# Performance work log

Measured on AMD Instinct MI355X. Metric: run time of the kernel, lower is better.

## Reference

```python
import jax, jax.numpy as jnp
import numpy as np
import math

H, D = 8, 128            # num_heads, head_dim (hidden=1024)
CHUNK, PAST, FUT = 12, 12, 0
CTX = CHUNK + PAST + FUT  # 24
SOFTCAP = 50.0
INVALID = 1e-09
Q_SCALE = D ** (-0.5) / math.log(2)
K_SCALE = math.log(1.0 + math.e) / math.log(2)


def setup_inputs() -> dict:
    key = jax.random.key(0)
    ks = jax.random.split(key, 7)
    B, S, HS = 16, 2400, 1024
    w = lambda k: jax.random.normal(k, (HS, HS), jnp.float32) * 0.02
    return {
        "x": jax.random.normal(ks[0], (B, S, HS), jnp.float32),
        "pos_emb": jax.random.normal(ks[1], (CTX + 1, HS), jnp.float32),
        "Wq": w(ks[2]),
        "Wk": w(ks[3]),
        "Wv": w(ks[4]),
        "Wpost": w(ks[5]),
        "Wrel": w(ks[6]),
        "per_dim_scale": jnp.zeros((D,), jnp.float32),
    }


def _to_blocks(t):
    # [B,S,H,D] -> [B,nb,CHUNK,H,D] (pad S up to multiple of CHUNK)
    B, S, h, d = t.shape
    nb = -(-S // CHUNK)
    t = jnp.pad(t, ((0, 0), (0, nb * CHUNK - S), (0, 0), (0, 0)))
    return t.reshape(B, nb, CHUNK, h, d)


def _block_context(t):
    # [B,S,H,D] -> [B,nb,CTX,H,D]: per-block window of PAST left context + chunk + FUT
    B, S, h, d = t.shape
    nb = -(-S // CHUNK)
    tp = jnp.pad(t, ((0, 0), (PAST, FUT + CHUNK - 1), (0, 0), (0, 0)))
    idx = jnp.arange(nb)[:, None] * CHUNK + jnp.arange(CTX)[None, :]  # [nb,CTX]
    return tp[:, idx]  # gather -> [B,nb,CTX,H,D]


def _rel_shift(x):
    # [B,H,nb,CHUNK,P] -> [B,H,nb,CHUNK,CTX] via Transformer-XL reshape trick
    B, h, nb, bs, P = x.shape
    x = jnp.pad(x, ((0, 0), (0, 0), (0, 0), (0, 0), (0, CTX + 1 - P)))
    x = x.reshape(B, h, nb, bs * (CTX + 1))[..., : bs * CTX]
    return x.reshape(B, h, nb, bs, CTX)


def reference(x, pos_emb, Wq, Wk, Wv, Wpost, Wrel, per_dim_scale):
    B, S, HS = x.shape
    q = (x @ Wq).reshape(B, S, H, D) * Q_SCALE * jax.nn.softplus(per_dim_scale)
    k = (x @ Wk).reshape(B, S, H, D) * K_SCALE
    v = (x @ Wv).reshape(B, S, H, D)

    qb = _to_blocks(q)        # [B,nb,CHUNK,H,D]
    kc = _block_context(k)    # [B,nb,CTX,H,D]
    vc = _block_context(v)    # [B,nb,CTX,H,D]
    nb = qb.shape[1]

    rel_k = (pos_emb @ Wrel).reshape(-1, H, D)  # [P,H,D]

    # content-content scores: [B,H,nb,CHUNK,CTX]
    matrix_ac = jnp.einsum('bnqhd,bnkhd->bhnqk', qb, kc)
    # content-position scores with rel-shift: [B,H,nb,CHUNK,P] -> [...,CTX]
    matrix_bd = jnp.einsum('bnqhd,phd->bhnqp', qb, rel_k)
    matrix_bd = _rel_shift(matrix_bd)

    attn = jnp.tanh((matrix_ac + matrix_bd) / SOFTCAP) * SOFTCAP
    attn = jax.nn.softmax(attn, axis=-1)

    out = jnp.einsum('bhnqk,bnkhd->bnqhd', attn, vc)  # [B,nb,CHUNK,H,D]
    out = out.reshape(B, nb * CHUNK, H * D)[:, :S, :]
    return out @ Wpost
```

## Files before the change

### kernel.cpp

```cpp
#include <hip/hip_runtime.h>
#include <hip/hip_bf16.h>
#include <cmath>

#define AS_GLOBAL __attribute__((address_space(1)))
#define AS_LDS    __attribute__((address_space(3)))

typedef __attribute__((ext_vector_type(8))) short bf16x8;
typedef __attribute__((ext_vector_type(4))) float f32x4;
typedef unsigned short u16;

__device__ __forceinline__ u16 f2bf(float f) {
  union { __hip_bfloat16 h; u16 u; } cv;
  cv.h = __float2bfloat16(f);
  return cv.u;
}
__device__ __forceinline__ float bf2f(u16 u) {
  union { unsigned u32; float f; } v;
  v.u32 = ((unsigned)u) << 16;
  return v.f;
}


__global__ void k_f32_to_bf16(const float* __restrict__ in, u16* __restrict__ out, int n4) {
  int i = blockIdx.x * 256 + threadIdx.x;
  if (i >= n4) return;
  float4 v = ((const float4*)in)[i];
  ushort4 o;
  o.x = f2bf(v.x); o.y = f2bf(v.y); o.z = f2bf(v.z); o.w = f2bf(v.w);
  ((ushort4*)out)[i] = o;
}

__global__ void k_transpose_w(const float* __restrict__ in, u16* __restrict__ out) {
  __shared__ float tile[32][33];
  const int tx = threadIdx.x & 31;
  const int ty = threadIdx.x >> 5;
  const int x0 = blockIdx.x * 32, y0 = blockIdx.y * 32;
  #pragma unroll
  for (int i = 0; i < 32; i += 8)
    tile[ty + i][tx] = in[(size_t)(y0 + ty + i) * 1024 + x0 + tx];
  __syncthreads();
  #pragma unroll
  for (int i = 0; i < 32; i += 8)
    out[(size_t)(x0 + ty + i) * 1024 + y0 + tx] = f2bf(tile[tx][ty + i]);
}

__global__ void k_qscale(const float* __restrict__ pds, float* __restrict__ qs, float qscale_c) {
  int n = blockIdx.x * 256 + threadIdx.x;
  float s = pds[n & 127];
  qs[n] = qscale_c * log1pf(expf(s));
}

__global__ void k_relk(const float* __restrict__ pos, const u16* __restrict__ wrt,
                       u16* __restrict__ relkb) {
  __shared__ float prow[1024];
  const int tid = threadIdx.x;
  const int p = blockIdx.y;
  ((float4*)prow)[tid] = ((const float4*)(pos + (size_t)p * 1024))[tid];
  __syncthreads();
  int nn = blockIdx.x * 256 + tid;
  const u16* wr = wrt + (size_t)nn * 1024;
  float acc = 0.f;
  for (int kk = 0; kk < 1024; kk += 8) {
    ushort4 u0 = *(const ushort4*)(wr + kk);
    ushort4 u1 = *(const ushort4*)(wr + kk + 4);
    acc += bf2f(u0.x) * prow[kk + 0] + bf2f(u0.y) * prow[kk + 1]
         + bf2f(u0.z) * prow[kk + 2] + bf2f(u0.w) * prow[kk + 3]
         + bf2f(u1.x) * prow[kk + 4] + bf2f(u1.y) * prow[kk + 5]
         + bf2f(u1.z) * prow[kk + 6] + bf2f(u1.w) * prow[kk + 7];
  }
  relkb[(size_t)p * 1024 + nn] = f2bf(acc);
}


#define BAR() __builtin_amdgcn_s_barrier()
#define VMCNT(n) asm volatile("s_waitcnt vmcnt(" #n ")" ::: "memory")

#define STAGE(d, t)                                                                       \
  do {                                                                                    \
    const int koff_ = (t) << 6;                                                           \
    _Pragma("unroll")                                                                     \
    for (int j_ = 0; j_ < 4; ++j_) {                                                      \
      int f_ = tid + j_ * 512;                                                            \
      int r_ = f_ >> 3;                                                                   \
      int cs_ = ((f_ & 7) ^ (r_ & 7)) << 3;                                               \
      __builtin_amdgcn_global_load_lds(                                                   \
          (const AS_GLOBAL u16*)(A + (size_t)(m0 + r_) * K + koff_ + cs_),                \
          (AS_LDS u16*)&lds[d][0][f_ << 3], 16, 0, 0);                                    \
      __builtin_amdgcn_global_load_lds(                                                   \
          (const AS_GLOBAL u16*)(Bt + (size_t)(n0 + r_) * K + koff_ + cs_),               \
          (AS_LDS u16*)&lds[d][1][f_ << 3], 16, 0, 0);                                    \
    }                                                                                     \
  } while (0)

#define COMPUTE(d)                                                                        \
  do {                                                                                    \
    bf16x8 bfr_[4][2];                                                                    \
    _Pragma("unroll")                                                                     \
    for (int ni_ = 0; ni_ < 4; ++ni_) {                                                   \
      int brow_ = wn * 64 + ni_ * 16 + l16;                                               \
      int bb_ = brow_ * 64, bx_ = brow_ & 7;                                              \
      bfr_[ni_][0] = *(const bf16x8*)&lds[d][1][bb_ + ((quad ^ bx_) << 3)];               \
      bfr_[ni_][1] = *(const bf16x8*)&lds[d][1][bb_ + (((4 + quad) ^ bx_) << 3)];         \
    }                                                                                     \
    __builtin_amdgcn_s_setprio(1);                                                        \
    _Pragma("unroll")                                                                     \
    for (int mi_ = 0; mi_ < 8; ++mi_) {                                                   \
      int arow_ = wm * 128 + mi_ * 16 + l16;                                              \
      int ab_ = arow_ * 64, ax_ = arow_ & 7;                                              \
      bf16x8 a0_ = *(const bf16x8*)&lds[d][0][ab_ + ((quad ^ ax_) << 3)];                 \
      bf16x8 a1_ = *(const bf16x8*)&lds[d][0][ab_ + (((4 + quad) ^ ax_) << 3)];           \
      _Pragma("unroll")                                                                   \
      for (int ni_ = 0; ni_ < 4; ++ni_) {                                                 \
        acc[mi_][ni_] =                                                                   \
            __builtin_amdgcn_mfma_f32_16x16x32_bf16(a0_, bfr_[ni_][0], acc[mi_][ni_], 0, 0, 0); \
        acc[mi_][ni_] =                                                                   \
            __builtin_amdgcn_mfma_f32_16x16x32_bf16(a1_, bfr_[ni_][1], acc[mi_][ni_], 0, 0, 0); \
      }                                                                                   \
    }                                                                                     \
    __builtin_amdgcn_s_setprio(0);                                                        \
  } while (0)

template <int OUTMODE>
__global__ __launch_bounds__(512, 2) void k_gemm256(
    const u16* __restrict__ A, const u16* __restrict__ Bt, void* __restrict__ Cout,
    const float* __restrict__ scale_vec, float scale_scalar, int M, int N, int K) {
  __shared__ __align__(16) u16 lds[2][2][16384];
  const int tid = threadIdx.x;
  const int wave = tid >> 6, lane = tid & 63;
  const int l16 = lane & 15, quad = lane >> 4;
  const int wm = wave >> 2, wn = wave & 3;

  const int q8 = (int)gridDim.x >> 3;
  const int wg = ((int)blockIdx.x & 7) * q8 + ((int)blockIdx.x >> 3);
  const int ntn = N >> 8;
  const int m0 = (wg / ntn) << 8;
  const int n0 = (wg % ntn) << 8;

  f32x4 acc[8][4];
  #pragma unroll
  for (int i = 0; i < 8; ++i)
    #pragma unroll
    for (int j = 0; j < 4; ++j) {
      f32x4 z = {0.f, 0.f, 0.f, 0.f};
      acc[i][j] = z;
    }

  STAGE(0, 0);
  STAGE(1, 1);
  VMCNT(8);
  BAR();

  const int nk = K >> 6;
  for (int i = 0; i + 2 < nk; i += 2) {
    COMPUTE(0);
    BAR();
    STAGE(0, i + 2);
    VMCNT(8);
    BAR();
    COMPUTE(1);
    BAR();
    STAGE(1, i + 3);
    VMCNT(8);
    BAR();
  }
  COMPUTE(0);
  VMCNT(0);
  BAR();
  COMPUTE(1);

  const int mb = m0 + wm * 128, nb = n0 + wn * 64;
  if (OUTMODE == 2) {
    u16* C = (u16*)Cout;
    #pragma unroll
    for (int ni = 0; ni < 4; ++ni) {
      int col = nb + ni * 16 + l16;
      #pragma unroll
      for (int mi = 0; mi < 8; ++mi) {
        int row = mb + mi * 16 + quad * 4;
        ushort4 o;
        o.x = f2bf(acc[mi][ni][0]);
        o.y = f2bf(acc[mi][ni][1]);
        o.z = f2bf(acc[mi][ni][2]);
        o.w = f2bf(acc[mi][ni][3]);
        *(ushort4*)&C[(size_t)col * M + row] = o;
      }
    }
  } else {
    #pragma unroll
    for (int ni = 0; ni < 4; ++ni) {
      int col = nb + ni * 16 + l16;
      float cs = scale_vec ? scale_vec[col] : scale_scalar;
      #pragma unroll
      for (int mi = 0; mi < 8; ++mi) {
        int row = mb + mi * 16 + quad * 4;
        #pragma unroll
        for (int r = 0; r < 4; ++r) {
          float v = acc[mi][ni][r] * cs;
          if (OUTMODE == 1)
            ((u16*)Cout)[(size_t)(row + r) * N + col] = f2bf(v);
          else
            ((float*)Cout)[(size_t)(row + r) * N + col] = v;
        }
      }
    }
  }
}

__global__ __launch_bounds__(256) void k_attn_mfma(
    const u16* __restrict__ q, const u16* __restrict__ k, const u16* __restrict__ vt,
    const u16* __restrict__ relkb, u16* __restrict__ ctx) {
  __shared__ float bdm_s[4][400];
  __shared__ u16 attnb[4][16 * 32];

  const int tid = threadIdx.x;
  const int w = tid >> 6, lane = tid & 63;
  const int l16 = lane & 15, quad = lane >> 4;
  const int id = blockIdx.x * 4 + w;
  const int b = id / 1600;
  const int rr = id % 1600;
  const int n = rr >> 3, h = rr & 7;
  const int s0 = n * 12;
  const size_t rowbase = (size_t)b * 2400;

  bf16x8 qf[4];
  {
    int sq = s0 + l16;
    if (sq > 2399) sq = 2399;
    const u16* qp = q + ((rowbase + sq) * 1024 + (size_t)h * 128 + quad * 8);
    #pragma unroll
    for (int c = 0; c < 4; ++c) qf[c] = *(const bf16x8*)(qp + 32 * c);
  }

  #pragma unroll
  for (int pt = 0; pt < 2; ++pt) {
    int p = pt * 16 + l16;
    const u16* rp = relkb + ((size_t)p * 1024 + (size_t)h * 128 + quad * 8);
    f32x4 acc = {0.f, 0.f, 0.f, 0.f};
    #pragma unroll
    for (int c = 0; c < 4; ++c)
      acc = __builtin_amdgcn_mfma_f32_16x16x32_bf16(qf[c], *(const bf16x8*)(rp + 32 * c), acc, 0, 0, 0);
    if (p < 25) {
      #pragma unroll
      for (int r = 0; r < 4; ++r)
        bdm_s[w][(quad * 4 + r) * 25 + p] = acc[r];
    }
  }
  __threadfence_block();

  float l0[4], l1[4];
  #pragma unroll
  for (int kt = 0; kt < 2; ++kt) {
    int t = kt * 16 + l16;
    int sk = s0 - 12 + t;
    bool kvalid = ((unsigned)sk < 2400u);
    int ska = kvalid ? sk : 0;
    const u16* kp = k + ((rowbase + ska) * 1024 + (size_t)h * 128 + quad * 8);
    short km = kvalid ? (short)0xFFFF : (short)0;
    bf16x8 kmv = {km, km, km, km, km, km, km, km};
    f32x4 acc = {0.f, 0.f, 0.f, 0.f};
    #pragma unroll
    for (int c = 0; c < 4; ++c) {
      bf16x8 kf = *(const bf16x8*)(kp + 32 * c);
      kf &= kmv;
      acc = __builtin_amdgcn_mfma_f32_16x16x32_bf16(qf[c], kf, acc, 0, 0, 0);
    }
    #pragma unroll
    for (int r = 0; r < 4; ++r) {
      float bd = bdm_s[w][(quad * 4 + r) * 24 + t];
      float lg = tanhf((acc[r] + bd) * (1.0f / 50.0f)) * 50.0f;
      if (kt == 1 && l16 >= 8) lg = -INFINITY;
      if (kt) l1[r] = lg; else l0[r] = lg;
    }
  }

  float at0[4], at1[4];
  #pragma unroll
  for (int r = 0; r < 4; ++r) {
    float m = fmaxf(l0[r], l1[r]);
    #pragma unroll
    for (int s = 1; s < 16; s <<= 1) m = fmaxf(m, __shfl_xor(m, s, 64));
    float e0 = __expf(l0[r] - m), e1 = __expf(l1[r] - m);
    float sum = e0 + e1;
    #pragma unroll
    for (int s = 1; s < 16; s <<= 1) sum += __shfl_xor(sum, s, 64);
    float inv = 1.0f / sum;
    at0[r] = e0 * inv;
    at1[r] = e1 * inv;
  }

  #pragma unroll
  for (int r = 0; r < 4; ++r) {
    attnb[w][(quad * 4 + r) * 32 + l16] = f2bf(at0[r]);
    attnb[w][(quad * 4 + r) * 32 + 16 + l16] = f2bf(at1[r]);
  }
  __threadfence_block();
  bf16x8 af = *(const bf16x8*)&attnb[w][l16 * 32 + quad * 8];

  int slo = s0 - 12 + quad * 8;
  bf16x8 vmsk;
  #pragma unroll
  for (int j = 0; j < 8; ++j)
    vmsk[j] = ((unsigned)(slo + j) < 2400u) ? (short)0xFFFF : (short)0;

  f32x4 oacc[8];
  #pragma unroll
  for (int dt = 0; dt < 8; ++dt) {
    int col = h * 128 + dt * 16 + l16;
    const u16* vp = vt + ((size_t)col * 38400 + (long)(rowbase + s0 - 12 + quad * 8));
    ushort4 va = *(const ushort4*)vp;
    ushort4 vb = *(const ushort4*)(vp + 4);
    bf16x8 vf = {(short)va.x, (short)va.y, (short)va.z, (short)va.w,
                 (short)vb.x, (short)vb.y, (short)vb.z, (short)vb.w};
    vf &= vmsk;
    f32x4 z = {0.f, 0.f, 0.f, 0.f};
    oacc[dt] = __builtin_amdgcn_mfma_f32_16x16x32_bf16(af, vf, z, 0, 0, 0);
  }

  if (quad < 3) {
    #pragma unroll
    for (int dt = 0; dt < 8; ++dt) {
      int col = h * 128 + dt * 16 + l16;
      #pragma unroll
      for (int r = 0; r < 4; ++r) {
        int qi = quad * 4 + r;
        ctx[(rowbase + s0 + qi) * 1024 + col] = f2bf(oacc[dt][r]);
      }
    }
  }
}


extern "C" void kernel_launch(void* const* d_in, const int* in_sizes, int n_in,
                              void* d_out, int out_size, void* d_ws, size_t ws_size,
                              hipStream_t stream) {
  const float* x       = (const float*)d_in[0];
  const float* pos_emb = (const float*)d_in[1];
  const float* Wq      = (const float*)d_in[2];
  const float* Wk      = (const float*)d_in[3];
  const float* Wv      = (const float*)d_in[4];
  const float* Wpost   = (const float*)d_in[5];
  const float* Wrel    = (const float*)d_in[6];
  const float* pds     = (const float*)d_in[7];
  float* out = (float*)d_out;

  const int M = 38400, HS = 1024;
  const size_t XE = (size_t)M * HS;

  u16* xbf = (u16*)d_ws;
  u16* qbf = xbf + XE;
  u16* kbf = qbf + XE;
  u16* vt_alloc = kbf + XE;
  u16* vt = vt_alloc + 16;
  u16* wqt = vt_alloc + XE + 64;
  u16* wkt = wqt + (size_t)HS * HS;
  u16* wvt = wkt + (size_t)HS * HS;
  u16* wrt = wvt + (size_t)HS * HS;
  u16* wpt = wrt + (size_t)HS * HS;
  u16* relkb = wpt + (size_t)HS * HS;
  float* qsc = (float*)(relkb + 32 * 1024);

  const double LN2 = 0.6931471805599453;
  const float QS = (float)((1.0 / sqrt(128.0)) / LN2);
  const float KS = (float)(log(1.0 + exp(1.0)) / LN2);

  k_f32_to_bf16<<<(int)(XE / 4 / 256), 256, 0, stream>>>(x, xbf, (int)(XE / 4));
  dim3 tg(32, 32);
  k_transpose_w<<<tg, 256, 0, stream>>>(Wq, wqt);
  k_transpose_w<<<tg, 256, 0, stream>>>(Wk, wkt);
  k_transpose_w<<<tg, 256, 0, stream>>>(Wv, wvt);
  k_transpose_w<<<tg, 256, 0, stream>>>(Wrel, wrt);
  k_transpose_w<<<tg, 256, 0, stream>>>(Wpost, wpt);
  k_qscale<<<4, 256, 0, stream>>>(pds, qsc, QS);
  k_relk<<<dim3(4, 25), 256, 0, stream>>>(pos_emb, wrt, relkb);
  const int NWG = (M / 256) * (HS / 256);
  k_gemm256<1><<<NWG, 512, 0, stream>>>(xbf, wqt, qbf, qsc, 1.0f, M, HS, HS);
  k_gemm256<1><<<NWG, 512, 0, stream>>>(xbf, wkt, kbf, nullptr, KS, M, HS, HS);
  k_gemm256<2><<<NWG, 512, 0, stream>>>(xbf, wvt, vt, nullptr, 1.0f, M, HS, HS);
  k_attn_mfma<<<25600 / 4, 256, 0, stream>>>(qbf, kbf, vt, relkb, xbf);
  k_gemm256<0><<<NWG, 512, 0, stream>>>(xbf, wpt, out, nullptr, 1.0f, M, HS, HS);
}
```

Baseline: 880.0 us.

## Restructure GEMM main loop into fine-grained interleaved load/MFMA quadrant schedule

The 256x256 GEMM main loop is rewritten so each K-tile is split into half-tile stages for A and B. LDS fragment loads, global-to-LDS staging and MFMA quadrant groups are interleaved with barriers and explicit vmcnt waits, in the style of a ping-pong schedule. The aim is to overlap global memory traffic with MFMA work at a finer grain than the previous whole-tile stage/compute alternation. The cost is many more barriers and a hand-tuned wait-count sequence that has to match the issue order exactly to stay correct.

New measurement: 862.3 us. 2.0% less time.

```diff
diff --git a/kernel.cpp b/kernel.cpp
--- a/kernel.cpp
+++ b/kernel.cpp
@@ -72,53 +72,42 @@
 }
 
 
-#define BAR() __builtin_amdgcn_s_barrier()
-#define VMCNT(n) asm volatile("s_waitcnt vmcnt(" #n ")" ::: "memory")
-
-#define STAGE(d, t)                                                                       \
-  do {                                                                                    \
-    const int koff_ = (t) << 6;                                                           \
-    _Pragma("unroll")                                                                     \
-    for (int j_ = 0; j_ < 4; ++j_) {                                                      \
-      int f_ = tid + j_ * 512;                                                            \
-      int r_ = f_ >> 3;                                                                   \
-      int cs_ = ((f_ & 7) ^ (r_ & 7)) << 3;                                               \
-      __builtin_amdgcn_global_load_lds(                                                   \
-          (const AS_GLOBAL u16*)(A + (size_t)(m0 + r_) * K + koff_ + cs_),                \
-          (AS_LDS u16*)&lds[d][0][f_ << 3], 16, 0, 0);                                    \
-      __builtin_amdgcn_global_load_lds(                                                   \
-          (const AS_GLOBAL u16*)(Bt + (size_t)(n0 + r_) * K + koff_ + cs_),               \
-          (AS_LDS u16*)&lds[d][1][f_ << 3], 16, 0, 0);                                    \
-    }                                                                                     \
-  } while (0)
-
-#define COMPUTE(d)                                                                        \
-  do {                                                                                    \
-    bf16x8 bfr_[4][2];                                                                    \
-    _Pragma("unroll")                                                                     \
-    for (int ni_ = 0; ni_ < 4; ++ni_) {                                                   \
-      int brow_ = wn * 64 + ni_ * 16 + l16;                                               \
-      int bb_ = brow_ * 64, bx_ = brow_ & 7;                                              \
-      bfr_[ni_][0] = *(const bf16x8*)&lds[d][1][bb_ + ((quad ^ bx_) << 3)];               \
-      bfr_[ni_][1] = *(const bf16x8*)&lds[d][1][bb_ + (((4 + quad) ^ bx_) << 3)];         \
-    }                                                                                     \
-    __builtin_amdgcn_s_setprio(1);                                                        \
-    _Pragma("unroll")                                                                     \
-    for (int mi_ = 0; mi_ < 8; ++mi_) {                                                   \
-      int arow_ = wm * 128 + mi_ * 16 + l16;                                              \
-      int ab_ = arow_ * 64, ax_ = arow_ & 7;                                              \
-      bf16x8 a0_ = *(const bf16x8*)&lds[d][0][ab_ + ((quad ^ ax_) << 3)];                 \
-      bf16x8 a1_ = *(const bf16x8*)&lds[d][0][ab_ + (((4 + quad) ^ ax_) << 3)];           \
-      _Pragma("unroll")                                                                   \
-      for (int ni_ = 0; ni_ < 4; ++ni_) {                                                 \
-        acc[mi_][ni_] =                                                                   \
-            __builtin_amdgcn_mfma_f32_16x16x32_bf16(a0_, bfr_[ni_][0], acc[mi_][ni_], 0, 0, 0); \
-        acc[mi_][ni_] =                                                                   \
-            __builtin_amdgcn_mfma_f32_16x16x32_bf16(a1_, bfr_[ni_][1], acc[mi_][ni_], 0, 0, 0); \
-      }                                                                                   \
-    }                                                                                     \
-    __builtin_amdgcn_s_setprio(0);                                                        \
-  } while (0)
+#define VMCNT(n) do { asm volatile("s_waitcnt vmcnt(" #n ")" ::: "memory"); \
+                      __builtin_amdgcn_sched_barrier(0); } while (0)
+#define BARF() do { asm volatile("" ::: "memory"); __builtin_amdgcn_s_barrier(); asm volatile("" ::: "memory"); } while (0)
+#define GLD(SRC, DST) __builtin_amdgcn_global_load_lds((const AS_GLOBAL u16*)(SRC), (AS_LDS u16*)(DST), 16, 0, 0)
+#define LDSA(d) ((AS_LDS char*)&lds[d][0][0])
+#define LDSB(d) ((AS_LDS char*)&lds[d][1][0])
+
+#define STAGE_A(d, h, t) do {                                                   \
+  GLD(sA0 + (((size_t)(h)) << 6) * K + ((t) << 6), LDSA(d) + dA0 + ((h) << 13)); \
+  GLD(sA1 + (((size_t)(h)) << 6) * K + ((t) << 6), LDSA(d) + dA1 + ((h) << 13)); \
+} while (0)
+#define STAGE_B(d, h, t) do {                                                   \
+  GLD(sB0 + (((size_t)(h)) << 5) * K + ((t) << 6), LDSB(d) + dB0 + ((h) << 12)); \
+  GLD(sB1 + (((size_t)(h)) << 5) * K + ((t) << 6), LDSB(d) + dB1 + ((h) << 12)); \
+} while (0)
+
+#define LOAD_A(d, qm) do {                                                       \
+  _Pragma("unroll") for (int mi_ = 0; mi_ < 4; ++mi_) {                          \
+    af[mi_][0] = *(const bf16x8*)&lds[d][0][abase + (((qm)*64 + mi_*16) << 6) + gk0]; \
+    af[mi_][1] = *(const bf16x8*)&lds[d][0][abase + (((qm)*64 + mi_*16) << 6) + gk1]; \
+  } } while (0)
+#define LOAD_B(d, qn) do {                                                       \
+  _Pragma("unroll") for (int ni_ = 0; ni_ < 2; ++ni_) {                          \
+    bfb[ni_][0] = *(const bf16x8*)&lds[d][1][bbase + (((qn)*32 + ni_*16) << 6) + gk0]; \
+    bfb[ni_][1] = *(const bf16x8*)&lds[d][1][bbase + (((qn)*32 + ni_*16) << 6) + gk1]; \
+  } } while (0)
+#define MFMA16(qm, qn) do {                                                      \
+  __builtin_amdgcn_s_setprio(1);                                                 \
+  _Pragma("unroll") for (int mi_ = 0; mi_ < 4; ++mi_)                            \
+  _Pragma("unroll") for (int ni_ = 0; ni_ < 2; ++ni_) {                          \
+    acc[(qm)*4+mi_][(qn)*2+ni_] = __builtin_amdgcn_mfma_f32_16x16x32_bf16(       \
+        af[mi_][0], bfb[ni_][0], acc[(qm)*4+mi_][(qn)*2+ni_], 0, 0, 0);          \
+    acc[(qm)*4+mi_][(qn)*2+ni_] = __builtin_amdgcn_mfma_f32_16x16x32_bf16(       \
+        af[mi_][1], bfb[ni_][1], acc[(qm)*4+mi_][(qn)*2+ni_], 0, 0, 0);          \
+  }                                                                              \
+  __builtin_amdgcn_s_setprio(0); } while (0)
 
 template <int OUTMODE>
 __global__ __launch_bounds__(512, 2) void k_gemm256(
@@ -136,6 +125,28 @@
   const int m0 = (wg / ntn) << 8;
   const int n0 = (wg % ntn) << 8;
 
+  const int sx = l16 & 7;
+  const int gk0 = (quad ^ sx) << 3;
+  const int gk1 = ((4 + quad) ^ sx) << 3;
+  const int abase = (wm * 128 + l16) << 6;
+  const int bbase = (wn * 64 + l16) << 6;
+
+  const int rl0 = tid >> 3, g0 = tid & 7;
+  const int rl1 = rl0 + 64;
+  const int swz0 = (g0 ^ (rl0 & 7)) << 3;
+  const int rbA0 = ((rl0 >> 6) << 7) + (rl0 & 63);
+  const int rbA1 = ((rl1 >> 6) << 7) + (rl1 & 63);
+  const int rbB0 = ((rl0 >> 5) << 6) + (rl0 & 31);
+  const int rbB1 = ((rl1 >> 5) << 6) + (rl1 & 31);
+  const u16* sA0 = A + (size_t)(m0 + rbA0) * K + swz0;
+  const u16* sA1 = A + (size_t)(m0 + rbA1) * K + swz0;
+  const u16* sB0 = Bt + (size_t)(n0 + rbB0) * K + swz0;
+  const u16* sB1 = Bt + (size_t)(n0 + rbB1) * K + swz0;
+  const int dA0 = (rbA0 << 7) + (g0 << 4);
+  const int dA1 = (rbA1 << 7) + (g0 << 4);
+  const int dB0 = (rbB0 << 7) + (g0 << 4);
+  const int dB1 = (rbB1 << 7) + (g0 << 4);
+
   f32x4 acc[8][4];
   #pragma unroll
   for (int i = 0; i < 8; ++i)
@@ -145,28 +156,67 @@
       acc[i][j] = z;
     }
 
-  STAGE(0, 0);
-  STAGE(1, 1);
-  VMCNT(8);
-  BAR();
+  bf16x8 af[4][2], bfb[2][2];
+
+  STAGE_B(0, 0, 0);
+  STAGE_A(0, 1, 0);
+  STAGE_A(0, 0, 0);
+  STAGE_B(0, 1, 0);
+  STAGE_B(1, 0, 1);
+  STAGE_A(1, 1, 1);
+  VMCNT(6);
+  BARF();
 
   const int nk = K >> 6;
-  for (int i = 0; i + 2 < nk; i += 2) {
-    COMPUTE(0);
-    BAR();
-    STAGE(0, i + 2);
-    VMCNT(8);
-    BAR();
-    COMPUTE(1);
-    BAR();
-    STAGE(1, i + 3);
-    VMCNT(8);
-    BAR();
-  }
-  COMPUTE(0);
-  VMCNT(0);
-  BAR();
-  COMPUTE(1);
+  for (int i = 0; i < (nk >> 1) - 1; ++i) {
+    const int t1 = 2 * i + 1, t2 = 2 * i + 2, t3 = 2 * i + 3;
+    LOAD_A(0, 0); LOAD_B(0, 0);
+    STAGE_A(1, 0, t1);
+    BARF(); MFMA16(0, 0); BARF();
+    LOAD_A(0, 1);
+    STAGE_B(1, 1, t1);
+    BARF(); MFMA16(1, 0); VMCNT(8); BARF();
+    LOAD_B(0, 1);
+    STAGE_B(0, 0, t2);
+    BARF(); MFMA16(1, 1); BARF();
+    LOAD_A(0, 0);
+    STAGE_A(0, 1, t2);
+    BARF(); MFMA16(0, 1); VMCNT(6); BARF();
+    LOAD_A(1, 0); LOAD_B(1, 0);
+    STAGE_A(0, 0, t2);
+    BARF(); MFMA16(0, 0); BARF();
+    LOAD_A(1, 1);
+    STAGE_B(0, 1, t2);
+    BARF(); MFMA16(1, 0); VMCNT(8); BARF();
+    LOAD_B(1, 1);
+    STAGE_B(1, 0, t3);
+    BARF(); MFMA16(1, 1); BARF();
+    LOAD_A(1, 0);
+    STAGE_A(1, 1, t3);
+    BARF(); MFMA16(0, 1); VMCNT(6); BARF();
+  }
+
+  {
+    const int t1 = nk - 1;
+    LOAD_A(0, 0); LOAD_B(0, 0);
+    STAGE_A(1, 0, t1);
+    BARF(); MFMA16(0, 0); BARF();
+    LOAD_A(0, 1);
+    STAGE_B(1, 1, t1);
+    BARF(); MFMA16(1, 0); VMCNT(8); BARF();
+    LOAD_B(0, 1);
+    BARF(); MFMA16(1, 1); BARF();
+    LOAD_A(0, 0);
+    BARF(); MFMA16(0, 1); VMCNT(2); BARF();
+    LOAD_A(1, 0); LOAD_B(1, 0);
+    BARF(); MFMA16(0, 0); BARF();
+    LOAD_A(1, 1);
+    BARF(); MFMA16(1, 0); VMCNT(0); BARF();
+    LOAD_B(1, 1);
+    BARF(); MFMA16(1, 1); BARF();
+    LOAD_A(1, 0);
+    BARF(); MFMA16(0, 1);
+  }
 
   const int mb = m0 + wm * 128, nb = n0 + wn * 64;
   if (OUTMODE == 2) {
@@ -206,6 +256,12 @@
   }
 }
 
+#undef STAGE_A
+#undef STAGE_B
+#undef LOAD_A
+#undef LOAD_B
+#undef MFMA16
+
 __global__ __launch_bounds__(256) void k_attn_mfma(
     const u16* __restrict__ q, const u16* __restrict__ k, const u16* __restrict__ vt,
     const u16* __restrict__ relkb, u16* __restrict__ ctx) {
```
